# Performance work log

Hardware: AMD Instinct MI355X
Metric: run time of the kernel (lower is better)

## Reference

```python
import jax, jax.numpy as jnp
import numpy as np

N_SRC = 200000
N_DST = 50000
N_EDGES = 1600000
D_IN = 256
D_OUT = 16


def setup_inputs() -> dict:
    key = jax.random.key(0)
    k1, k2, k3, k4, k5 = jax.random.split(key, 5)
    x = jax.random.normal(k1, (N_SRC, D_IN), dtype=jnp.float32)
    W = jax.random.normal(k2, (D_IN, D_OUT), dtype=jnp.float32) / np.sqrt(D_IN)
    b = jnp.zeros((D_OUT,), dtype=jnp.float32)
    edge_src = jax.random.randint(k3, (N_EDGES,), 0, N_SRC, dtype=jnp.int64)
    edge_dst = jax.random.randint(k4, (N_EDGES,), 0, N_DST, dtype=jnp.int64)
    res_n_id = jax.random.randint(k5, (N_DST,), 0, N_SRC, dtype=jnp.int64)
    return {"x": x, "W": W, "b": b, "edge_src": edge_src,
            "edge_dst": edge_dst, "res_n_id": res_n_id}


def reference(x, W, b, edge_src, edge_dst, res_n_id):
    n_src = x.shape[0]
    n_dst = res_n_id.shape[0]
    # Linear transform first (small out dim keeps edge-level traffic low).
    x_lin = x @ W                                   # [n_src, d_out]
    ones = jnp.ones(edge_src.shape, dtype=x.dtype)
    deg_src = jax.ops.segment_sum(ones, edge_src, num_segments=n_src)
    deg_dst = jax.ops.segment_sum(ones, edge_dst, num_segments=n_dst)
    # GCN symmetric normalization with self-loops (sampled bipartite block).
    norm = jax.lax.rsqrt((deg_src[edge_src] + 1.0) * (deg_dst[edge_dst] + 1.0))
    msgs = norm[:, None] * x_lin[edge_src]          # [E, d_out] irregular gather
    agg = jax.ops.segment_sum(msgs, edge_dst, num_segments=n_dst)
    # Self-loop term uses the gathered target-node features x[res_n_id].
    self_term = x_lin[res_n_id] / (deg_dst + 1.0)[:, None]
    out = agg + self_term + b                       # [n_dst, d_out]
    return jax.nn.log_softmax(out, axis=1)
```

## Files before the change

kernel.cpp:

```cpp
#include <hip/hip_runtime.h>
#include <hip/hip_bf16.h>

#define D_IN   256
#define D_OUT  16

__device__ __forceinline__ void acc4(float4& a, float xs, const float4& wv) {
  a.x += xs * wv.x; a.y += xs * wv.y; a.z += xs * wv.z; a.w += xs * wv.w;
}

__global__ __launch_bounds__(256) void xlin_deg_kernel(
    const float* __restrict__ x, const float* __restrict__ W,
    float* __restrict__ xlin, const int* __restrict__ es,
    float* __restrict__ deg_src,
    int n_src, int n_edges, int stride, int nblocks) {
  const int kg = threadIdx.x & 15;
  const int cg = (threadIdx.x >> 4) & 3;
  const int wv = threadIdx.x >> 6;
  const int gw = blockIdx.x * 4 + wv;
  const int total_waves = nblocks * 4;

  float4 wf[4][4];
#pragma unroll
  for (int j = 0; j < 4; ++j)
#pragma unroll
    for (int jj = 0; jj < 4; ++jj) {
      int r = 4 * kg + 64 * j + jj;
      wf[j][jj] = *reinterpret_cast<const float4*>(W + r * D_OUT + cg * 4);
    }

  const int npairs = n_src >> 1;
  for (int p = gw; p < npairs; p += total_waves) {
    const int r0 = 2 * p, r1 = 2 * p + 1;
    float4 xv0[4], xv1[4];
#pragma unroll
    for (int j = 0; j < 4; ++j) {
      xv0[j] = *reinterpret_cast<const float4*>(x + (size_t)r0 * D_IN + (kg + 16 * j) * 4);
      xv1[j] = *reinterpret_cast<const float4*>(x + (size_t)r1 * D_IN + (kg + 16 * j) * 4);
    }
    float4 a0 = make_float4(0.f, 0.f, 0.f, 0.f);
    float4 a1 = make_float4(0.f, 0.f, 0.f, 0.f);
#pragma unroll
    for (int j = 0; j < 4; ++j) {
      acc4(a0, xv0[j].x, wf[j][0]); acc4(a1, xv1[j].x, wf[j][0]);
      acc4(a0, xv0[j].y, wf[j][1]); acc4(a1, xv1[j].y, wf[j][1]);
      acc4(a0, xv0[j].z, wf[j][2]); acc4(a1, xv1[j].z, wf[j][2]);
      acc4(a0, xv0[j].w, wf[j][3]); acc4(a1, xv1[j].w, wf[j][3]);
    }
#pragma unroll
    for (int off = 1; off < 16; off <<= 1) {
      a0.x += __shfl_xor(a0.x, off, 16); a0.y += __shfl_xor(a0.y, off, 16);
      a0.z += __shfl_xor(a0.z, off, 16); a0.w += __shfl_xor(a0.w, off, 16);
      a1.x += __shfl_xor(a1.x, off, 16); a1.y += __shfl_xor(a1.y, off, 16);
      a1.z += __shfl_xor(a1.z, off, 16); a1.w += __shfl_xor(a1.w, off, 16);
    }
    if (kg == 0) {
      *reinterpret_cast<float4*>(xlin + (size_t)r0 * D_OUT + cg * 4) = a0;
      *reinterpret_cast<float4*>(xlin + (size_t)r1 * D_OUT + cg * 4) = a1;
    }
  }

  for (int e = blockIdx.x * 256 + threadIdx.x; e < n_edges; e += nblocks * 256) {
    int s = es[(size_t)e * stride];
    atomicAdd(&deg_src[s], 1.0f);
  }
}

__global__ __launch_bounds__(256) void edge_kernel(
    const int* __restrict__ es, const int* __restrict__ ed,
    const float* __restrict__ xlin, const float* __restrict__ deg_src,
    float* __restrict__ m, float* __restrict__ deg_dst,
    int n_edges, int stride) {
  int t = blockIdx.x * 256 + threadIdx.x;
  int e = t >> 4;
  int c = t & 15;
  if (e >= n_edges) return;
  int s = es[(size_t)e * stride];
  int d = ed[(size_t)e * stride];
  float v = rsqrtf(deg_src[s] + 1.0f) * xlin[(size_t)s * D_OUT + c];
  atomicAdd(&m[(size_t)d * D_OUT + c], v);
  if (c == 0) atomicAdd(&deg_dst[d], 1.0f);
}

__global__ __launch_bounds__(256) void finalize_kernel(
    const float* __restrict__ xlin, const int* __restrict__ rn,
    const float* __restrict__ deg_dst, const float* __restrict__ b,
    float* __restrict__ out, int n_dst, int stride) {
  int t = blockIdx.x * 256 + threadIdx.x;
  int row = t >> 4;
  int c = t & 15;
  if (row >= n_dst) return;
  int r = rn[(size_t)row * stride];
  float dd = deg_dst[row];
  float v = out[(size_t)row * D_OUT + c] * rsqrtf(dd + 1.0f)
          + xlin[(size_t)r * D_OUT + c] / (dd + 1.0f)
          + b[c];
  float mx = v;
#pragma unroll
  for (int off = 1; off < 16; off <<= 1) mx = fmaxf(mx, __shfl_xor(mx, off, 16));
  float ex = expf(v - mx);
  float sum = ex;
#pragma unroll
  for (int off = 1; off < 16; off <<= 1) sum += __shfl_xor(sum, off, 16);
  out[(size_t)row * D_OUT + c] = v - mx - logf(sum);
}

extern "C" void kernel_launch(void* const* d_in, const int* in_sizes, int n_in,
                              void* d_out, int out_size, void* d_ws, size_t ws_size,
                              hipStream_t stream) {
  const float* x  = (const float*)d_in[0];
  const float* W  = (const float*)d_in[1];
  const float* b  = (const float*)d_in[2];
  const int*   es = (const int*)d_in[3];
  const int*   ed = (const int*)d_in[4];
  const int*   rn = (const int*)d_in[5];
  float* out = (float*)d_out;

  const int n_src = in_sizes[0] / D_IN;
  const int n_dst = out_size / D_OUT;

  int stride_e = 1, n_e = in_sizes[3];
  if (in_sizes[3] == 3200000) { stride_e = 2; n_e = 1600000; }
  int stride_r = 1;
  if (in_sizes[5] == 2 * n_dst) { stride_r = 2; }

  float* xlin    = (float*)d_ws;
  float* deg_src = xlin + (size_t)n_src * D_OUT;
  float* deg_dst = deg_src + n_src;

  (void)hipMemsetAsync(deg_src, 0, (size_t)(n_src + n_dst) * sizeof(float), stream);
  (void)hipMemsetAsync(d_out, 0, (size_t)out_size * sizeof(float), stream);

  {
    const int grid = 2048;
    xlin_deg_kernel<<<grid, 256, 0, stream>>>(x, W, xlin, es, deg_src,
                                              n_src, n_e, stride_e, grid);
  }
  {
    long long threads = (long long)n_e * D_OUT;
    int grid = (int)((threads + 255) / 256);
    edge_kernel<<<grid, 256, 0, stream>>>(es, ed, xlin, deg_src, out, deg_dst,
                                          n_e, stride_e);
  }
  {
    int threads = n_dst * D_OUT;
    int grid = (threads + 255) / 256;
    finalize_kernel<<<grid, 256, 0, stream>>>(xlin, rn, deg_dst, b, out, n_dst, stride_r);
  }
}
```

Before: 513.3 us.

## Specialize blocks into GEMV and degree-counting roles, move dst degree count out

The first kernel now splits its grid: 768 blocks compute x@W while the remaining blocks count both source and destination degrees with atomics. Destination degree counting moves out of the per-edge-channel edge kernel, which removes one atomic per edge from that kernel. The aim is to overlap the memory-bound GEMV with the atomic-bound degree histogram and to lighten the edge kernel. The fixed split ratio could leave one role idle if the two workloads are unbalanced.

```diff
diff --git a/kernel.cpp b/kernel.cpp
--- a/kernel.cpp
+++ b/kernel.cpp
@@ -10,66 +10,72 @@
 
 __global__ __launch_bounds__(256) void xlin_deg_kernel(
     const float* __restrict__ x, const float* __restrict__ W,
-    float* __restrict__ xlin, const int* __restrict__ es,
-    float* __restrict__ deg_src,
-    int n_src, int n_edges, int stride, int nblocks) {
-  const int kg = threadIdx.x & 15;
-  const int cg = (threadIdx.x >> 4) & 3;
-  const int wv = threadIdx.x >> 6;
-  const int gw = blockIdx.x * 4 + wv;
-  const int total_waves = nblocks * 4;
+    float* __restrict__ xlin,
+    const int* __restrict__ es, const int* __restrict__ ed,
+    float* __restrict__ deg_src, float* __restrict__ deg_dst,
+    int n_src, int n_edges, int stride, int nb_gemv, int nblocks) {
+  if (blockIdx.x < (unsigned)nb_gemv) {
+    const int kg = threadIdx.x & 15;
+    const int cg = (threadIdx.x >> 4) & 3;
+    const int wv = threadIdx.x >> 6;
+    const int gw = blockIdx.x * 4 + wv;
+    const int total_waves = nb_gemv * 4;
 
-  float4 wf[4][4];
+    float4 wf[4][4];
 #pragma unroll
-  for (int j = 0; j < 4; ++j)
+    for (int j = 0; j < 4; ++j)
 #pragma unroll
-    for (int jj = 0; jj < 4; ++jj) {
-      int r = 4 * kg + 64 * j + jj;
-      wf[j][jj] = *reinterpret_cast<const float4*>(W + r * D_OUT + cg * 4);
+      for (int jj = 0; jj < 4; ++jj) {
+        int r = 4 * kg + 64 * j + jj;
+        wf[j][jj] = *reinterpret_cast<const float4*>(W + r * D_OUT + cg * 4);
+      }
+
+    const int npairs = n_src >> 1;
+    for (int p = gw; p < npairs; p += total_waves) {
+      const int r0 = 2 * p, r1 = 2 * p + 1;
+      float4 xv0[4], xv1[4];
+#pragma unroll
+      for (int j = 0; j < 4; ++j) {
+        xv0[j] = *reinterpret_cast<const float4*>(x + (size_t)r0 * D_IN + (kg + 16 * j) * 4);
+        xv1[j] = *reinterpret_cast<const float4*>(x + (size_t)r1 * D_IN + (kg + 16 * j) * 4);
+      }
+      float4 a0 = make_float4(0.f, 0.f, 0.f, 0.f);
+      float4 a1 = make_float4(0.f, 0.f, 0.f, 0.f);
+#pragma unroll
+      for (int j = 0; j < 4; ++j) {
+        acc4(a0, xv0[j].x, wf[j][0]); acc4(a1, xv1[j].x, wf[j][0]);
+        acc4(a0, xv0[j].y, wf[j][1]); acc4(a1, xv1[j].y, wf[j][1]);
+        acc4(a0, xv0[j].z, wf[j][2]); acc4(a1, xv1[j].z, wf[j][2]);
+        acc4(a0, xv0[j].w, wf[j][3]); acc4(a1, xv1[j].w, wf[j][3]);
+      }
+#pragma unroll
+      for (int off = 1; off < 16; off <<= 1) {
+        a0.x += __shfl_xor(a0.x, off, 16); a0.y += __shfl_xor(a0.y, off, 16);
+        a0.z += __shfl_xor(a0.z, off, 16); a0.w += __shfl_xor(a0.w, off, 16);
+        a1.x += __shfl_xor(a1.x, off, 16); a1.y += __shfl_xor(a1.y, off, 16);
+        a1.z += __shfl_xor(a1.z, off, 16); a1.w += __shfl_xor(a1.w, off, 16);
+      }
+      if (kg == 0) {
+        *reinterpret_cast<float4*>(xlin + (size_t)r0 * D_OUT + cg * 4) = a0;
+        *reinterpret_cast<float4*>(xlin + (size_t)r1 * D_OUT + cg * 4) = a1;
+      }
     }
-
-  const int npairs = n_src >> 1;
-  for (int p = gw; p < npairs; p += total_waves) {
-    const int r0 = 2 * p, r1 = 2 * p + 1;
-    float4 xv0[4], xv1[4];
-#pragma unroll
-    for (int j = 0; j < 4; ++j) {
-      xv0[j] = *reinterpret_cast<const float4*>(x + (size_t)r0 * D_IN + (kg + 16 * j) * 4);
-      xv1[j] = *reinterpret_cast<const float4*>(x + (size_t)r1 * D_IN + (kg + 16 * j) * 4);
+  } else {
+    const int nb_h = nblocks - nb_gemv;
+    const int t0 = (blockIdx.x - nb_gemv) * 256 + threadIdx.x;
+    for (int e = t0; e < n_edges; e += nb_h * 256) {
+      int s = es[(size_t)e * stride];
+      int d = ed[(size_t)e * stride];
+      atomicAdd(&deg_src[s], 1.0f);
+      atomicAdd(&deg_dst[d], 1.0f);
     }
-    float4 a0 = make_float4(0.f, 0.f, 0.f, 0.f);
-    float4 a1 = make_float4(0.f, 0.f, 0.f, 0.f);
-#pragma unroll
-    for (int j = 0; j < 4; ++j) {
-      acc4(a0, xv0[j].x, wf[j][0]); acc4(a1, xv1[j].x, wf[j][0]);
-      acc4(a0, xv0[j].y, wf[j][1]); acc4(a1, xv1[j].y, wf[j][1]);
-      acc4(a0, xv0[j].z, wf[j][2]); acc4(a1, xv1[j].z, wf[j][2]);
-      acc4(a0, xv0[j].w, wf[j][3]); acc4(a1, xv1[j].w, wf[j][3]);
-    }
-#pragma unroll
-    for (int off = 1; off < 16; off <<= 1) {
-      a0.x += __shfl_xor(a0.x, off, 16); a0.y += __shfl_xor(a0.y, off, 16);
-      a0.z += __shfl_xor(a0.z, off, 16); a0.w += __shfl_xor(a0.w, off, 16);
-      a1.x += __shfl_xor(a1.x, off, 16); a1.y += __shfl_xor(a1.y, off, 16);
-      a1.z += __shfl_xor(a1.z, off, 16); a1.w += __shfl_xor(a1.w, off, 16);
-    }
-    if (kg == 0) {
-      *reinterpret_cast<float4*>(xlin + (size_t)r0 * D_OUT + cg * 4) = a0;
-      *reinterpret_cast<float4*>(xlin + (size_t)r1 * D_OUT + cg * 4) = a1;
-    }
-  }
-
-  for (int e = blockIdx.x * 256 + threadIdx.x; e < n_edges; e += nblocks * 256) {
-    int s = es[(size_t)e * stride];
-    atomicAdd(&deg_src[s], 1.0f);
   }
 }
 
 __global__ __launch_bounds__(256) void edge_kernel(
     const int* __restrict__ es, const int* __restrict__ ed,
     const float* __restrict__ xlin, const float* __restrict__ deg_src,
-    float* __restrict__ m, float* __restrict__ deg_dst,
-    int n_edges, int stride) {
+    float* __restrict__ m, int n_edges, int stride) {
   int t = blockIdx.x * 256 + threadIdx.x;
   int e = t >> 4;
   int c = t & 15;
@@ -78,7 +84,6 @@
   int d = ed[(size_t)e * stride];
   float v = rsqrtf(deg_src[s] + 1.0f) * xlin[(size_t)s * D_OUT + c];
   atomicAdd(&m[(size_t)d * D_OUT + c], v);
-  if (c == 0) atomicAdd(&deg_dst[d], 1.0f);
 }
 
 __global__ __launch_bounds__(256) void finalize_kernel(
@@ -131,15 +136,16 @@
   (void)hipMemsetAsync(d_out, 0, (size_t)out_size * sizeof(float), stream);
 
   {
-    const int grid = 2048;
-    xlin_deg_kernel<<<grid, 256, 0, stream>>>(x, W, xlin, es, deg_src,
-                                              n_src, n_e, stride_e, grid);
+    const int nb_gemv = 768, nblocks = 2048;
+    xlin_deg_kernel<<<nblocks, 256, 0, stream>>>(x, W, xlin, es, ed,
+                                                 deg_src, deg_dst,
+                                                 n_src, n_e, stride_e,
+                                                 nb_gemv, nblocks);
   }
   {
     long long threads = (long long)n_e * D_OUT;
     int grid = (int)((threads + 255) / 256);
-    edge_kernel<<<grid, 256, 0, stream>>>(es, ed, xlin, deg_src, out, deg_dst,
-                                          n_e, stride_e);
+    edge_kernel<<<grid, 256, 0, stream>>>(es, ed, xlin, deg_src, out, n_e, stride_e);
   }
   {
     int threads = n_dst * D_OUT;
```

Result: slower. 530.5 us (+3.3%).
